# Kernel optimization log

Measured on AMD Instinct MI355X. Metric: run time of the kernel, lower is better.

The kernel has to match this reference:

```python
import jax, jax.numpy as jnp
import numpy as np

HEADS = 16

def setup_inputs() -> dict:
    key = jax.random.key(0)
    k1, k2, k3 = jax.random.split(key, 3)
    B, N, C = 4, 4096, 1024
    x = jax.random.normal(k1, (B, N, C), dtype=jnp.float32)
    w_qkv = jax.random.normal(k2, (3 * C, C), dtype=jnp.float32) * (C ** -0.5)
    w_proj = jax.random.normal(k3, (C, C), dtype=jnp.float32) * (C ** -0.5)
    b_proj = jnp.zeros((C,), dtype=jnp.float32)
    return {"x": x, "w_qkv": w_qkv, "w_proj": w_proj, "b_proj": b_proj}

def reference(x, w_qkv, w_proj, b_proj):
    B, N, C = x.shape
    H = HEADS
    D = C // H
    qkv = x @ w_qkv.T                      # [B,N,3C]
    q, k, v = jnp.split(qkv, 3, axis=-1)   # each [B,N,C]
    # b n (h d) -> b h d n
    def to_bhdn(t):
        return t.reshape(B, N, H, D).transpose(0, 2, 3, 1)
    q = jax.nn.relu(to_bhdn(q))
    k = jax.nn.relu(to_bhdn(k))
    v = to_bhdn(v)
    eps = jnp.finfo(q.dtype).eps
    ksum = k.sum(axis=-1)                                   # [B,H,D]
    z = 1.0 / (jnp.einsum('bhd,bhdn->bhn', ksum, q) + eps)  # [B,H,N]
    context = jnp.einsum('bhdn,bhen->bhde', v, k)            # v @ k^T, [B,H,D,D]
    out = jnp.einsum('bhde,bhen->bhdn', context, q)          # [B,H,D,N]
    out = out * z[:, :, None, :]
    # b h d n -> b n (h d)
    out = out.transpose(0, 3, 1, 2).reshape(B, N, C)
    return out @ w_proj.T + b_proj
```

## Files before the change

kernel.cpp:

```cpp
#include <hip/hip_runtime.h>
#include <hip/hip_bf16.h>


typedef __bf16 bf16;
typedef __bf16 bf16x8 __attribute__((ext_vector_type(8)));
typedef __bf16 bf16x4 __attribute__((ext_vector_type(4)));
typedef float  f32x4  __attribute__((ext_vector_type(4)));

#define MFMA16(a, b, c) __builtin_amdgcn_mfma_f32_16x16x32_bf16((a), (b), (c), 0, 0, 0)

__device__ __forceinline__ void gload_lds16(const bf16* g, bf16* l) {
  __builtin_amdgcn_global_load_lds(
      (const __attribute__((address_space(1))) void*)g,
      (__attribute__((address_space(3))) void*)l, 16, 0, 0);
}

__global__ __launch_bounds__(256) void cvt_f32_bf16(const float* __restrict__ src,
                                                    bf16* __restrict__ dst, long n) {
  const long stride4 = (long)gridDim.x * blockDim.x * 4;
  for (long j = ((long)blockIdx.x * blockDim.x + threadIdx.x) * 4; j < n; j += stride4) {
    const float4 v = *(const float4*)(src + j);
    bf16x4 o;
    o[0] = (bf16)v.x; o[1] = (bf16)v.y; o[2] = (bf16)v.z; o[3] = (bf16)v.w;
    *(bf16x4*)(dst + j) = o;
  }
}

template <int LDC, typename CO>
__global__ __launch_bounds__(512, 2) void gemm256(const bf16* __restrict__ A,
                                                  const bf16* __restrict__ Bm,
                                                  CO* __restrict__ Co,
                                                  const float* __restrict__ bias,
                                                  const int reluRows) {
  __shared__ bf16 As[2][256 * 64];
  __shared__ bf16 Bs[2][256 * 64];
  const int tid  = threadIdx.x;
  const int lane = tid & 63;
  const int w    = tid >> 6;
  const int wm   = w >> 2;
  const int wn   = w & 3;

  const int gx = gridDim.x, gy = gridDim.y;
  const int nwg = gx * gy;
  const int id  = blockIdx.x + gx * blockIdx.y;
  const int sid = (id & 7) * (nwg >> 3) + (id >> 3);
  int bx, by;
  if (gx < gy) { bx = sid % gx; by = sid / gx; }
  else         { by = sid % gy; bx = sid / gy; }
  const int i0 = by * 256;
  const int j0 = bx * 256;

  const int lr = lane >> 3;
  const int lc = (lane & 7) ^ lr;
  const bf16* Agl = A  + (long)(i0 + 8 * w + lr) * 1024 + lc * 8;
  const bf16* Bgl = Bm + (long)(j0 + 8 * w + lr) * 1024 + lc * 8;
  const int wofs = w * 512;

  const int r15 = lane & 15, g = lane >> 4;
  const int ck[2] = { ((0 + g) ^ (r15 & 7)) * 8, ((4 + g) ^ (r15 & 7)) * 8 };
  const int arow = (wm * 128 + r15) * 64;
  const int brow = (wn * 64 + r15) * 64;

  f32x4 acc[8][4] = {};

#pragma unroll
  for (int q = 0; q < 4; ++q) {
    gload_lds16(Agl + q * 65536, &As[0][q * 4096 + wofs]);
    gload_lds16(Bgl + q * 65536, &Bs[0][q * 4096 + wofs]);
  }

  for (int kt = 0; kt < 16; ++kt) {
    const int cur = kt & 1;
    if (kt < 15) {
      const long ko = (long)(kt + 1) * 64;
#pragma unroll
      for (int q = 0; q < 4; ++q) {
        gload_lds16(Agl + ko + q * 65536, &As[cur ^ 1][q * 4096 + wofs]);
        gload_lds16(Bgl + ko + q * 65536, &Bs[cur ^ 1][q * 4096 + wofs]);
      }
      asm volatile("s_waitcnt vmcnt(8)" ::: "memory");
    } else {
      asm volatile("s_waitcnt vmcnt(0)" ::: "memory");
    }
    __builtin_amdgcn_s_barrier();
    __builtin_amdgcn_sched_barrier(0);

    const bf16* Ab = &As[cur][arow];
    const bf16* Bb = &Bs[cur][brow];
#pragma unroll
    for (int ks = 0; ks < 2; ++ks) {
      bf16x8 af[8], bfr[4];
#pragma unroll
      for (int fm = 0; fm < 8; ++fm)
        af[fm] = *(const bf16x8*)(Ab + fm * 1024 + ck[ks]);
#pragma unroll
      for (int fn = 0; fn < 4; ++fn)
        bfr[fn] = *(const bf16x8*)(Bb + fn * 1024 + ck[ks]);
      __builtin_amdgcn_s_setprio(1);
#pragma unroll
      for (int fm = 0; fm < 8; ++fm)
#pragma unroll
        for (int fn = 0; fn < 4; ++fn)
          acc[fm][fn] = MFMA16(af[fm], bfr[fn], acc[fm][fn]);
      __builtin_amdgcn_s_setprio(0);
    }
    asm volatile("s_waitcnt lgkmcnt(0)" ::: "memory");
    __builtin_amdgcn_sched_barrier(0);
    __builtin_amdgcn_s_barrier();
  }

  const bool doRelu = (i0 < reluRows);
#pragma unroll
  for (int fm = 0; fm < 8; ++fm) {
    const int r0 = i0 + wm * 128 + fm * 16 + g * 4;
#pragma unroll
    for (int fn = 0; fn < 4; ++fn) {
      const int cc = j0 + wn * 64 + fn * 16 + r15;
      const float bv = bias ? bias[cc] : 0.0f;
#pragma unroll
      for (int jj = 0; jj < 4; ++jj) {
        float v = acc[fm][fn][jj] + bv;
        if (doRelu) v = fmaxf(v, 0.0f);
        Co[(long)(r0 + jj) * LDC + cc] = (CO)v;
      }
    }
  }
}

__global__ __launch_bounds__(256) void ctx_kernel(const bf16* __restrict__ QKV,
                                                  float* __restrict__ ctx_part,
                                                  float* __restrict__ ksum_part) {
  const int bh = blockIdx.x;
  const int s  = blockIdx.y;
  const int b  = bh >> 4, h = bh & 15;
  const int tid = threadIdx.x, lane = tid & 63, w = tid >> 6;
  const long ldq = 16384;
  const bf16* Kp = QKV + (long)(1024 + h * 64) * ldq + b * 4096 + s * 512;
  const bf16* Vp = QKV + (long)(2048 + h * 64) * ldq + b * 4096 + s * 512;

  const int r15  = lane & 15;
  const int koff = (lane >> 4) * 8;

  f32x4 acc[4] = {};
#pragma unroll 4
  for (int n = 0; n < 512; n += 32) {
    const bf16x8 a = *(const bf16x8*)(Vp + (long)(w * 16 + r15) * ldq + n + koff);
#pragma unroll
    for (int u = 0; u < 4; ++u) {
      const bf16x8 kb = *(const bf16x8*)(Kp + (long)(u * 16 + r15) * ldq + n + koff);
      acc[u] = MFMA16(a, kb, acc[u]);
    }
  }
  float* cp = ctx_part + (long)(bh * 8 + s) * 4096;
#pragma unroll
  for (int u = 0; u < 4; ++u)
#pragma unroll
    for (int jj = 0; jj < 4; ++jj) {
      const int d = w * 16 + (lane >> 4) * 4 + jj;
      const int e = u * 16 + r15;
      cp[d * 64 + e] = acc[u][jj];
    }

  const int e = tid >> 2, q4 = tid & 3;
  const bf16* kr = Kp + (long)e * ldq + q4 * 128;
  float sum = 0.0f;
#pragma unroll
  for (int i = 0; i < 128; i += 8) {
    const bf16x8 v = *(const bf16x8*)(kr + i);
#pragma unroll
    for (int jj = 0; jj < 8; ++jj) sum += (float)v[jj];
  }
  sum += __shfl_xor(sum, 1);
  sum += __shfl_xor(sum, 2);
  if (q4 == 0) ksum_part[(bh * 8 + s) * 64 + e] = sum;
}

__global__ __launch_bounds__(256) void out_kernel(const bf16* __restrict__ QKV,
                                                  const float* __restrict__ ctx_part,
                                                  const float* __restrict__ ksum_part,
                                                  bf16* __restrict__ O) {
  __shared__ bf16 ctx_lds[64 * 88];
  __shared__ bf16 qlds[256 * 80];
  __shared__ float ksum_lds[64];
  __shared__ float zlds[256];

  const int nc = blockIdx.x;
  const int bh = blockIdx.y;
  const int b = bh >> 4, h = bh & 15;
  const int tid = threadIdx.x, lane = tid & 63, w = tid >> 6;
  const int n0 = nc * 256;
  const long ldq = 16384;

  const float* cp = ctx_part + (long)bh * 8 * 4096;
#pragma unroll
  for (int r = 0; r < 16; ++r) {
    const int idx = tid + r * 256;
    float v = 0.0f;
#pragma unroll
    for (int s2 = 0; s2 < 8; ++s2) v += cp[s2 * 4096 + idx];
    ctx_lds[(idx >> 6) * 88 + (idx & 63)] = (bf16)v;
  }
  if (tid < 64) {
    float v = 0.0f;
#pragma unroll
    for (int s2 = 0; s2 < 8; ++s2) v += ksum_part[(bh * 8 + s2) * 64 + tid];
    ksum_lds[tid] = v;
  }
  {
    const bf16* Qp = QKV + (long)(h * 64) * ldq + b * 4096 + n0;
    const int e = tid >> 2, seg = tid & 3;
    const bf16* qr = Qp + (long)e * ldq + seg * 64;
#pragma unroll
    for (int i = 0; i < 64; i += 8) {
      const bf16x8 v = *(const bf16x8*)(qr + i);
#pragma unroll
      for (int jj = 0; jj < 8; ++jj) qlds[(seg * 64 + i + jj) * 80 + e] = v[jj];
    }
  }
  __syncthreads();

  {
    float a = 0.0f;
    const bf16* qrow = qlds + tid * 80;
#pragma unroll
    for (int d = 0; d < 64; ++d) a += (float)qrow[d] * ksum_lds[d];
    zlds[tid] = 1.0f / (a + 1.1920929e-07f);
  }
  const int r15 = lane & 15;
  const int koff = (lane >> 4) * 8;
  bf16x8 afr[4][2];
#pragma unroll
  for (int t = 0; t < 4; ++t)
#pragma unroll
    for (int s2 = 0; s2 < 2; ++s2)
      afr[t][s2] = *(const bf16x8*)(ctx_lds + (t * 16 + r15) * 88 + s2 * 32 + koff);
  __syncthreads();

#pragma unroll
  for (int nt = 0; nt < 4; ++nt) {
    const int ntile = w * 4 + nt;
    bf16x8 bfr[2];
#pragma unroll
    for (int s2 = 0; s2 < 2; ++s2)
      bfr[s2] = *(const bf16x8*)(qlds + (ntile * 16 + r15) * 80 + s2 * 32 + koff);
    f32x4 accn[4] = {};
#pragma unroll
    for (int t = 0; t < 4; ++t) {
      accn[t] = MFMA16(afr[t][0], bfr[0], accn[t]);
      accn[t] = MFMA16(afr[t][1], bfr[1], accn[t]);
    }
    const int ncol = n0 + ntile * 16 + r15;
    const float zv = zlds[ntile * 16 + r15];
    bf16* orow = O + (long)(b * 4096 + ncol) * 1024 + h * 64;
#pragma unroll
    for (int t = 0; t < 4; ++t) {
      const int d0 = t * 16 + (lane >> 4) * 4;
      bf16x4 pk;
#pragma unroll
      for (int jj = 0; jj < 4; ++jj) pk[jj] = (bf16)(accn[t][jj] * zv);
      *(bf16x4*)(orow + d0) = pk;
    }
  }
}

extern "C" void kernel_launch(void* const* d_in, const int* in_sizes, int n_in,
                              void* d_out, int out_size, void* d_ws, size_t ws_size,
                              hipStream_t stream) {
  const float* x      = (const float*)d_in[0];
  const float* w_qkv  = (const float*)d_in[1];
  const float* w_proj = (const float*)d_in[2];
  const float* b_proj = (const float*)d_in[3];
  float* out = (float*)d_out;

  char* ws = (char*)d_ws;
  bf16*  QKV       = (bf16*)ws;
  float* ctx_part  = (float*)(ws + 100663296);
  float* ksum_part = (float*)(ws + 100663296 + 8388608);
  bf16*  xb        = (bf16*)(ws + 109182976);
  bf16*  O         = xb;
  bf16*  wqkvb     = (bf16*)(ws + 109182976 + 33554432);
  bf16*  wprojb    = (bf16*)(ws + 109182976 + 33554432 + 6291456);

  cvt_f32_bf16<<<2048, 256, 0, stream>>>(x,      xb,     16777216);
  cvt_f32_bf16<<<512,  256, 0, stream>>>(w_qkv,  wqkvb,  3145728);
  cvt_f32_bf16<<<256,  256, 0, stream>>>(w_proj, wprojb, 1048576);
  gemm256<16384, bf16><<<dim3(64, 12), 512, 0, stream>>>(wqkvb, xb, QKV, nullptr, 2048);
  ctx_kernel<<<dim3(64, 8), 256, 0, stream>>>(QKV, ctx_part, ksum_part);
  out_kernel<<<dim3(16, 64), 256, 0, stream>>>(QKV, ctx_part, ksum_part, O);
  gemm256<1024, float><<<dim3(4, 64), 512, 0, stream>>>(O, wprojb, out, b_proj, 0);
}
```

Baseline: 262.9 us.

## Split GEMM K-tile into halves with interleaved staging and MFMA phases

Restructures the bf16 GEMM main loop so each 64-wide K tile is stored as two 32-wide halves with a new swizzled LDS layout. Global-to-LDS loads for the next tile are issued in four small chunks interleaved between MFMA phases, with barriers arranged in a ping-pong schedule. The aim is finer-grained overlap of memory traffic with matrix math and fewer register-held fragments at once. It adds many more barriers per iteration and relies on subtle vmcnt accounting.

New measurement: 272.4 us. +3.6%, slower.

```diff
diff --git a/kernel.cpp b/kernel.cpp
--- a/kernel.cpp
+++ b/kernel.cpp
@@ -26,14 +26,19 @@
   }
 }
 
+__device__ __forceinline__ bf16x8 ldfrag(const bf16* half_, int row, int g) {
+  const int off = ((row >> 1) << 6) + (((((row & 1) << 2) | g) ^ ((row >> 1) & 7)) << 3);
+  return *(const bf16x8*)(half_ + off);
+}
+
 template <int LDC, typename CO>
 __global__ __launch_bounds__(512, 2) void gemm256(const bf16* __restrict__ A,
                                                   const bf16* __restrict__ Bm,
                                                   CO* __restrict__ Co,
                                                   const float* __restrict__ bias,
                                                   const int reluRows) {
-  __shared__ bf16 As[2][256 * 64];
-  __shared__ bf16 Bs[2][256 * 64];
+  __shared__ bf16 As[2][2][8192];
+  __shared__ bf16 Bs[2][2][8192];
   const int tid  = threadIdx.x;
   const int lane = tid & 63;
   const int w    = tid >> 6;
@@ -50,64 +55,108 @@
   const int i0 = by * 256;
   const int j0 = bx * 256;
 
-  const int lr = lane >> 3;
-  const int lc = (lane & 7) ^ lr;
-  const bf16* Agl = A  + (long)(i0 + 8 * w + lr) * 1024 + lc * 8;
-  const bf16* Bgl = Bm + (long)(j0 + 8 * w + lr) * 1024 + lc * 8;
-  const int wofs = w * 512;
+  const int q3   = (lane & 7) ^ (lane >> 3);
+  const int row0 = 2 * (w * 8 + (lane >> 3)) + (q3 >> 2);
+  const int c0   = q3 & 3;
+  const bf16* Asrc = A  + (long)(i0 + row0) * 1024 + c0 * 8;
+  const bf16* Bsrc = Bm + (long)(j0 + row0) * 1024 + c0 * 8;
+  bf16* AldsW[2][2] = { { &As[0][0][w * 512], &As[0][1][w * 512] },
+                        { &As[1][0][w * 512], &As[1][1][w * 512] } };
+  bf16* BldsW[2][2] = { { &Bs[0][0][w * 512], &Bs[0][1][w * 512] },
+                        { &Bs[1][0][w * 512], &Bs[1][1][w * 512] } };
 
   const int r15 = lane & 15, g = lane >> 4;
-  const int ck[2] = { ((0 + g) ^ (r15 & 7)) * 8, ((4 + g) ^ (r15 & 7)) * 8 };
-  const int arow = (wm * 128 + r15) * 64;
-  const int brow = (wn * 64 + r15) * 64;
+  const int arow = wm * 128 + r15;
+  const int brow = wn * 64 + r15;
 
   f32x4 acc[8][4] = {};
 
-#pragma unroll
-  for (int q = 0; q < 4; ++q) {
-    gload_lds16(Agl + q * 65536, &As[0][q * 4096 + wofs]);
-    gload_lds16(Bgl + q * 65536, &Bs[0][q * 4096 + wofs]);
-  }
-
-  for (int kt = 0; kt < 16; ++kt) {
-    const int cur = kt & 1;
-    if (kt < 15) {
-      const long ko = (long)(kt + 1) * 64;
-#pragma unroll
-      for (int q = 0; q < 4; ++q) {
-        gload_lds16(Agl + ko + q * 65536, &As[cur ^ 1][q * 4096 + wofs]);
-        gload_lds16(Bgl + ko + q * 65536, &Bs[cur ^ 1][q * 4096 + wofs]);
-      }
-      asm volatile("s_waitcnt vmcnt(8)" ::: "memory");
-    } else {
-      asm volatile("s_waitcnt vmcnt(0)" ::: "memory");
-    }
-    __builtin_amdgcn_s_barrier();
-    __builtin_amdgcn_sched_barrier(0);
-
-    const bf16* Ab = &As[cur][arow];
-    const bf16* Bb = &Bs[cur][brow];
-#pragma unroll
-    for (int ks = 0; ks < 2; ++ks) {
-      bf16x8 af[8], bfr[4];
-#pragma unroll
-      for (int fm = 0; fm < 8; ++fm)
-        af[fm] = *(const bf16x8*)(Ab + fm * 1024 + ck[ks]);
-#pragma unroll
-      for (int fn = 0; fn < 4; ++fn)
-        bfr[fn] = *(const bf16x8*)(Bb + fn * 1024 + ck[ks]);
-      __builtin_amdgcn_s_setprio(1);
-#pragma unroll
-      for (int fm = 0; fm < 8; ++fm)
-#pragma unroll
-        for (int fn = 0; fn < 4; ++fn)
-          acc[fm][fn] = MFMA16(af[fm], bfr[fn], acc[fm][fn]);
-      __builtin_amdgcn_s_setprio(0);
-    }
+#define STAGE_HALF(srcb, ldsw, kt, kh)                                   \
+  do {                                                                   \
+    const bf16* s_ = (srcb) + (kt) * 64 + (kh) * 32;                     \
+    gload_lds16(s_,           (ldsw));                                   \
+    gload_lds16(s_ + 131072,  (ldsw) + 4096);                            \
+  } while (0)
+
+  STAGE_HALF(Asrc, AldsW[0][0], 0, 0);
+  STAGE_HALF(Bsrc, BldsW[0][0], 0, 0);
+  STAGE_HALF(Asrc, AldsW[0][1], 0, 1);
+  STAGE_HALF(Bsrc, BldsW[0][1], 0, 1);
+  asm volatile("s_waitcnt vmcnt(4)" ::: "memory");
+  __builtin_amdgcn_s_barrier();
+
+  for (int t = 0; t < 16; ++t) {
+    const int d = t & 1, e = d ^ 1;
+    bf16x8 af[8], bf0, bf1;
+
+#pragma unroll
+    for (int fm = 0; fm < 8; ++fm) af[fm] = ldfrag(&As[d][0][0], arow + fm * 16, g);
+    bf0 = ldfrag(&Bs[d][0][0], brow + 0 * 16, g);
+    bf1 = ldfrag(&Bs[d][0][0], brow + 1 * 16, g);
+    if (t < 15) STAGE_HALF(Asrc, AldsW[e][0], t + 1, 0);
+    __builtin_amdgcn_s_barrier();
     asm volatile("s_waitcnt lgkmcnt(0)" ::: "memory");
     __builtin_amdgcn_sched_barrier(0);
-    __builtin_amdgcn_s_barrier();
-  }
+    __builtin_amdgcn_s_setprio(1);
+#pragma unroll
+    for (int fm = 0; fm < 8; ++fm) {
+      acc[fm][0] = MFMA16(af[fm], bf0, acc[fm][0]);
+      acc[fm][1] = MFMA16(af[fm], bf1, acc[fm][1]);
+    }
+    __builtin_amdgcn_s_setprio(0);
+    __builtin_amdgcn_s_barrier();
+
+    bf0 = ldfrag(&Bs[d][0][0], brow + 2 * 16, g);
+    bf1 = ldfrag(&Bs[d][0][0], brow + 3 * 16, g);
+    if (t < 15) STAGE_HALF(Bsrc, BldsW[e][0], t + 1, 0);
+    __builtin_amdgcn_s_barrier();
+    asm volatile("s_waitcnt lgkmcnt(0)" ::: "memory");
+    __builtin_amdgcn_sched_barrier(0);
+    __builtin_amdgcn_s_setprio(1);
+#pragma unroll
+    for (int fm = 0; fm < 8; ++fm) {
+      acc[fm][2] = MFMA16(af[fm], bf0, acc[fm][2]);
+      acc[fm][3] = MFMA16(af[fm], bf1, acc[fm][3]);
+    }
+    __builtin_amdgcn_s_setprio(0);
+    if (t < 15) { asm volatile("s_waitcnt vmcnt(4)" ::: "memory"); }
+    else        { asm volatile("s_waitcnt vmcnt(0)" ::: "memory"); }
+    __builtin_amdgcn_s_barrier();
+
+#pragma unroll
+    for (int fm = 0; fm < 8; ++fm) af[fm] = ldfrag(&As[d][1][0], arow + fm * 16, g);
+    bf0 = ldfrag(&Bs[d][1][0], brow + 0 * 16, g);
+    bf1 = ldfrag(&Bs[d][1][0], brow + 1 * 16, g);
+    if (t < 15) STAGE_HALF(Asrc, AldsW[e][1], t + 1, 1);
+    __builtin_amdgcn_s_barrier();
+    asm volatile("s_waitcnt lgkmcnt(0)" ::: "memory");
+    __builtin_amdgcn_sched_barrier(0);
+    __builtin_amdgcn_s_setprio(1);
+#pragma unroll
+    for (int fm = 0; fm < 8; ++fm) {
+      acc[fm][0] = MFMA16(af[fm], bf0, acc[fm][0]);
+      acc[fm][1] = MFMA16(af[fm], bf1, acc[fm][1]);
+    }
+    __builtin_amdgcn_s_setprio(0);
+    __builtin_amdgcn_s_barrier();
+
+    bf0 = ldfrag(&Bs[d][1][0], brow + 2 * 16, g);
+    bf1 = ldfrag(&Bs[d][1][0], brow + 3 * 16, g);
+    if (t < 15) STAGE_HALF(Bsrc, BldsW[e][1], t + 1, 1);
+    __builtin_amdgcn_s_barrier();
+    asm volatile("s_waitcnt lgkmcnt(0)" ::: "memory");
+    __builtin_amdgcn_sched_barrier(0);
+    __builtin_amdgcn_s_setprio(1);
+#pragma unroll
+    for (int fm = 0; fm < 8; ++fm) {
+      acc[fm][2] = MFMA16(af[fm], bf0, acc[fm][2]);
+      acc[fm][3] = MFMA16(af[fm], bf1, acc[fm][3]);
+    }
+    __builtin_amdgcn_s_setprio(0);
+    if (t < 15) { asm volatile("s_waitcnt vmcnt(4)" ::: "memory"); }
+    __builtin_amdgcn_s_barrier();
+  }
+#undef STAGE_HALF
 
   const bool doRelu = (i0 < reluRows);
 #pragma unroll
```

## Merge conversion kernels and replace QKV GEMM with smaller-tile single-buffered kernel

Applied to the files above, without the earlier changes.

The three fp32-to-bf16 conversion launches become one kernel that walks a combined index range, saving two launches. The QKV projection now uses a new 128x128 tile GEMM with 256 threads and a 32-wide K step, single-buffered LDS and no software pipelining, in place of the 256x256 double-buffered kernel. This gives many more workgroups (3072 instead of 768), but each tile gets less reuse and every K step waits on two barriers with no overlap of loads and compute.

After: 266.6 us. No clear change (+1.4%).

```diff
diff --git a/kernel.cpp b/kernel.cpp
--- a/kernel.cpp
+++ b/kernel.cpp
@@ -15,14 +15,93 @@
       (__attribute__((address_space(3))) void*)l, 16, 0, 0);
 }
 
-__global__ __launch_bounds__(256) void cvt_f32_bf16(const float* __restrict__ src,
-                                                    bf16* __restrict__ dst, long n) {
-  const long stride4 = (long)gridDim.x * blockDim.x * 4;
-  for (long j = ((long)blockIdx.x * blockDim.x + threadIdx.x) * 4; j < n; j += stride4) {
-    const float4 v = *(const float4*)(src + j);
+__global__ __launch_bounds__(256) void cvt3(const float* __restrict__ x,  bf16* __restrict__ xb,
+                                            const float* __restrict__ wq, bf16* __restrict__ wqb,
+                                            const float* __restrict__ wp, bf16* __restrict__ wpb) {
+  const long stride = (long)gridDim.x * 256;
+  for (long i4 = (long)blockIdx.x * 256 + threadIdx.x; i4 < 5242880; i4 += stride) {
+    const float* s; bf16* d; long off;
+    if (i4 < 4194304)      { s = x;  d = xb;  off = i4; }
+    else if (i4 < 4980736) { s = wq; d = wqb; off = i4 - 4194304; }
+    else                   { s = wp; d = wpb; off = i4 - 4980736; }
+    const float4 v = *(const float4*)(s + off * 4);
     bf16x4 o;
     o[0] = (bf16)v.x; o[1] = (bf16)v.y; o[2] = (bf16)v.z; o[3] = (bf16)v.w;
-    *(bf16x4*)(dst + j) = o;
+    *(bf16x4*)(d + off * 4) = o;
+  }
+}
+
+template <int LDC, typename CO>
+__global__ __launch_bounds__(256) void gemm_bt(const bf16* __restrict__ A,
+                                               const bf16* __restrict__ Bm,
+                                               CO* __restrict__ Co,
+                                               const float* __restrict__ bias,
+                                               const int reluRows) {
+  __shared__ bf16 As[128 * 32];
+  __shared__ bf16 Bs[128 * 32];
+  const int tid  = threadIdx.x;
+  const int lane = tid & 63;
+  const int w    = tid >> 6;
+  const int wr   = w >> 1;
+  const int wc   = w & 1;
+
+  const int gx = gridDim.x, gy = gridDim.y;
+  const int nwg = gx * gy;
+  const int id  = blockIdx.x + gx * blockIdx.y;
+  const int sid = (nwg & 7) ? id : ((id & 7) * (nwg >> 3) + (id >> 3));
+  const int j0 = (sid % gx) * 128;
+  const int i0 = (sid / gx) * 128;
+
+  const int srow = lane >> 2;
+  const int scol = (lane & 3) * 8;
+  const bf16* Ag = A  + (long)(i0 + w * 32 + srow) * 1024 + scol;
+  const bf16* Bg = Bm + (long)(j0 + w * 32 + srow) * 1024 + scol;
+  bf16* Asw = As + w * 32 * 32;
+  bf16* Bsw = Bs + w * 32 * 32;
+
+  const int r15  = lane & 15;
+  const int koff = (lane >> 4) * 8;
+
+  f32x4 acc[4][4] = {};
+
+  for (int kk = 0; kk < 1024; kk += 32) {
+    gload_lds16(Ag + kk,             Asw);
+    gload_lds16(Ag + kk + 16 * 1024, Asw + 16 * 32);
+    gload_lds16(Bg + kk,             Bsw);
+    gload_lds16(Bg + kk + 16 * 1024, Bsw + 16 * 32);
+    __syncthreads();
+    bf16x8 af[4], bfm[4];
+#pragma unroll
+    for (int t = 0; t < 4; ++t)
+      af[t] = *(const bf16x8*)(As + (wr * 64 + t * 16 + r15) * 32 + koff);
+#pragma unroll
+    for (int u = 0; u < 4; ++u)
+      bfm[u] = *(const bf16x8*)(Bs + (wc * 64 + u * 16 + r15) * 32 + koff);
+#pragma unroll
+    for (int t = 0; t < 4; ++t)
+#pragma unroll
+      for (int u = 0; u < 4; ++u)
+        acc[t][u] = MFMA16(af[t], bfm[u], acc[t][u]);
+    __syncthreads();
+  }
+
+  const bool doRelu = (i0 < reluRows);
+  const int rbase = i0 + wr * 64;
+  const int cbase = j0 + wc * 64;
+#pragma unroll
+  for (int t = 0; t < 4; ++t) {
+    const int r0 = rbase + t * 16 + (lane >> 4) * 4;
+#pragma unroll
+    for (int u = 0; u < 4; ++u) {
+      const int cc = cbase + u * 16 + r15;
+      const float bv = bias ? bias[cc] : 0.0f;
+#pragma unroll
+      for (int jj = 0; jj < 4; ++jj) {
+        float v = acc[t][u][jj] + bv;
+        if (doRelu) v = fmaxf(v, 0.0f);
+        Co[(long)(r0 + jj) * LDC + cc] = (CO)v;
+      }
+    }
   }
 }
 
@@ -281,10 +360,8 @@
   bf16*  wqkvb     = (bf16*)(ws + 109182976 + 33554432);
   bf16*  wprojb    = (bf16*)(ws + 109182976 + 33554432 + 6291456);
 
-  cvt_f32_bf16<<<2048, 256, 0, stream>>>(x,      xb,     16777216);
-  cvt_f32_bf16<<<512,  256, 0, stream>>>(w_qkv,  wqkvb,  3145728);
-  cvt_f32_bf16<<<256,  256, 0, stream>>>(w_proj, wprojb, 1048576);
-  gemm256<16384, bf16><<<dim3(64, 12), 512, 0, stream>>>(wqkvb, xb, QKV, nullptr, 2048);
+  cvt3<<<2048, 256, 0, stream>>>(x, xb, w_qkv, wqkvb, w_proj, wprojb);
+  gemm_bt<16384, bf16><<<dim3(128, 24), 256, 0, stream>>>(wqkvb, xb, QKV, nullptr, 2048);
   ctx_kernel<<<dim3(64, 8), 256, 0, stream>>>(QKV, ctx_part, ksum_part);
   out_kernel<<<dim3(16, 64), 256, 0, stream>>>(QKV, ctx_part, ksum_part, O);
   gemm256<1024, float><<<dim3(4, 64), 512, 0, stream>>>(O, wprojb, out, b_proj, 0);
```
